# Kernel optimization log

Measured on AMD Instinct MI355X. Metric: run time of the kernel, lower is better.

## Reference

```python
import jax, jax.numpy as jnp
import numpy as np

N = 100000   # nodes
E = 1600000  # edges (before self-loops)
HIDDEN = 256
BN_EPS = 1e-5


def setup_inputs() -> dict:
    key = jax.random.key(0)
    ks = jax.random.split(key, 16)
    def lin(k, i, o):
        return jax.random.normal(k, (i, o), jnp.float32) / np.float32(np.sqrt(i))
    inp = {
        "x": jax.random.normal(ks[0], (N, 21), jnp.float32),
        "edge_index": jax.random.randint(ks[1], (2, E), 0, N),
        # GCNConv weights (stored [in, out]) + biases
        "W1": lin(ks[2], 21, HIDDEN), "b1": jnp.zeros((HIDDEN,), jnp.float32),
        "W2": lin(ks[3], HIDDEN, 112), "b2": jnp.zeros((112,), jnp.float32),
        # dense MLP
        "lin2_w": lin(ks[4], 112, 256), "lin2_b": jnp.zeros((256,), jnp.float32),
        "lin3_w": lin(ks[5], 256, 100), "lin3_b": jnp.zeros((100,), jnp.float32),
        "lin4_w": lin(ks[6], 100, 1),   "lin4_b": jnp.zeros((1,), jnp.float32),
        # batchnorm affine params
        "g1": jnp.ones((112,), jnp.float32), "be1": jnp.zeros((112,), jnp.float32),
        "g2": jnp.ones((256,), jnp.float32), "be2": jnp.zeros((256,), jnp.float32),
        "g3": jnp.ones((100,), jnp.float32), "be3": jnp.zeros((100,), jnp.float32),
    }
    return inp


def _gcn_conv(x, W, b, src, dst, n):
    # PyG GCNConv: h = xW; out_i = sum_j norm_ij * h_j (+ bias), sym-normalized w/ self-loops
    h = x @ W                                              # [N, C]
    deg = jax.ops.segment_sum(jnp.ones(src.shape, h.dtype), dst, num_segments=n)
    dinv = jnp.where(deg > 0, jax.lax.rsqrt(deg), 0.0)
    norm = dinv[src] * dinv[dst]                            # [E']
    out = jax.ops.segment_sum(h[src] * norm[:, None], dst, num_segments=n)
    return out + b


def _bn(x, g, b):
    # train-mode batchnorm: biased batch variance
    m = jnp.mean(x, axis=0)
    v = jnp.mean(jnp.square(x - m), axis=0)
    return (x - m) * jax.lax.rsqrt(v + BN_EPS) * g + b


def reference(x, edge_index, W1, b1, W2, b2, lin2_w, lin2_b, lin3_w, lin3_b,
              lin4_w, lin4_b, g1, be1, g2, be2, g3, be3):
    n = x.shape[0]
    loops = jnp.arange(n, dtype=edge_index.dtype)
    src = jnp.concatenate([edge_index[0], loops])
    dst = jnp.concatenate([edge_index[1], loops])
    h = jax.nn.relu(_gcn_conv(x, W1, b1, src, dst, n))
    h = _gcn_conv(h, W2, b2, src, dst, n)
    h = jax.nn.relu(_bn(h, g1, be1))
    # dropout: identity (eval / deterministic)
    h = jax.nn.relu(_bn(h @ lin2_w + lin2_b, g2, be2))
    h = jax.nn.relu(_bn(h @ lin3_w + lin3_b, g3, be3))
    return h @ lin4_w + lin4_b
```

## Files before the change

### kernel.cpp

```cpp
#include <hip/hip_runtime.h>

#define N_NODES 100000
#define N_EDGES 1600000

typedef _Float16 f16x8 __attribute__((ext_vector_type(8)));
typedef _Float16 f16x4 __attribute__((ext_vector_type(4)));
typedef float fx4 __attribute__((ext_vector_type(4)));

#define NREP 16
#define NBUCK 196
#define CHUNK 8192
#define BCAP 12288

__global__ __launch_bounds__(256) void k_bin(const int* __restrict__ ei,
                                             unsigned* __restrict__ binned,
                                             int* __restrict__ gcount) {
  __shared__ unsigned pr[CHUNK];
  __shared__ unsigned srt[CHUNK];
  __shared__ unsigned char bk[CHUNK];
  __shared__ int hist[256], scanb[256], offs[256], bs[256], gb[256];
  const int t = threadIdx.x;
  const int e0 = blockIdx.x * CHUNK;
  const int n = min(CHUNK, N_EDGES - e0);
  hist[t] = 0;
  __syncthreads();
  for (int i = t; i < n; i += 256) {
    int src = ei[e0 + i], dst = ei[N_EDGES + e0 + i];
    int b = dst >> 9;
    pr[i] = ((unsigned)src << 9) | (unsigned)(dst & 511);
    bk[i] = (unsigned char)b;
    atomicAdd(&hist[b], 1);
  }
  __syncthreads();
  int v = hist[t];
  scanb[t] = v;
  __syncthreads();
  for (int off = 1; off < 256; off <<= 1) {
    int a = (t >= off) ? scanb[t - off] : 0;
    __syncthreads();
    scanb[t] += a;
    __syncthreads();
  }
  offs[t] = scanb[t] - v;
  bs[t] = scanb[t] - v;
  __syncthreads();
  for (int i = t; i < n; i += 256) {
    int b = bk[i];
    int p = atomicAdd(&offs[b], 1);
    srt[p] = pr[i];
  }
  if (t < NBUCK && v > 0) gb[t] = atomicAdd(&gcount[t], v);
  __syncthreads();
  int wave = t >> 6, lane = t & 63;
  for (int b = wave; b < NBUCK; b += 4) {
    int c = hist[b];
    if (c == 0) continue;
    int ls = bs[b], base = gb[b];
    unsigned* dstp = binned + (size_t)b * BCAP + base;
    for (int i = lane; i < c; i += 64) dstp[i] = srt[ls + i];
  }
}

__global__ void k_bscan(const int* __restrict__ gcount, int* __restrict__ gbase) {
  __shared__ int s[256];
  int t = threadIdx.x;
  int v = (t < NBUCK) ? gcount[t] : 0;
  s[t] = v;
  __syncthreads();
  for (int off = 1; off < 256; off <<= 1) {
    int a = (t >= off) ? s[t - off] : 0;
    __syncthreads();
    s[t] += a;
    __syncthreads();
  }
  if (t < NBUCK) gbase[t] = s[t] - v;
}

__global__ __launch_bounds__(256) void k_csr(const unsigned* __restrict__ binned,
                                             const int* __restrict__ gcount,
                                             const int* __restrict__ gbase,
                                             int* __restrict__ rowoff,
                                             int* __restrict__ cnt,
                                             float* __restrict__ dinv,
                                             int* __restrict__ csr) {
  __shared__ int hist[512], offs[512], ps[256];
  __shared__ unsigned srt[BCAP];
  const int b = blockIdx.x, t = threadIdx.x;
  const int n = min(gcount[b], BCAP);
  const int gb0 = gbase[b];
  const unsigned* bp = binned + (size_t)b * BCAP;
  hist[t] = 0;
  hist[t + 256] = 0;
  __syncthreads();
  for (int i = t; i < n; i += 256) atomicAdd(&hist[bp[i] & 511], 1);
  __syncthreads();
  int e0v = hist[2 * t], e1v = hist[2 * t + 1];
  ps[t] = e0v + e1v;
  __syncthreads();
  for (int off = 1; off < 256; off <<= 1) {
    int a = (t >= off) ? ps[t - off] : 0;
    __syncthreads();
    ps[t] += a;
    __syncthreads();
  }
  int excl = ps[t] - (e0v + e1v);
  offs[2 * t] = excl;
  offs[2 * t + 1] = excl + e0v;
  __syncthreads();
#pragma unroll
  for (int u = 0; u < 2; ++u) {
    int j = 2 * t + u;
    int nd = (b << 9) + j;
    if (nd < N_NODES) {
      int c = hist[j];
      cnt[nd] = c;
      dinv[nd] = rsqrtf((float)(c + 1));
      rowoff[nd] = gb0 + offs[j];
    }
  }
  __syncthreads();
  for (int i = t; i < n; i += 256) {
    unsigned p = bp[i];
    int d = p & 511;
    int pos = atomicAdd(&offs[d], 1);
    srt[pos] = p >> 9;
  }
  __syncthreads();
  for (int i = t; i < n; i += 256) csr[gb0 + i] = (int)srt[i];
}

__global__ void k_xpad(const float* __restrict__ x, const float* __restrict__ dinv,
                       float* __restrict__ xs) {
  int idx = blockIdx.x * 256 + threadIdx.x;
  if (idx >= N_NODES * 24) return;
  int r = idx / 24, c = idx - r * 24;
  xs[idx] = (c < 21) ? x[r * 21 + c] * dinv[r] : 0.f;
}

__global__ __launch_bounds__(256) void k_aggx(
    const float4* __restrict__ xs4, const float* __restrict__ dinv,
    const int* __restrict__ rowoff, const int* __restrict__ cnt,
    const int* __restrict__ csr, float4* __restrict__ aggx4) {
  int lane = threadIdx.x & 63, wave = threadIdx.x >> 6;
  int j = lane / 6, c4 = lane - j * 6;
  if (j >= 10) return;
  int i = blockIdx.x * 40 + wave * 10 + j;
  float di = dinv[i];
  int start = rowoff[i], len = cnt[i];
  float4 a0 = xs4[i * 6 + c4];
  float4 a1 = make_float4(0.f, 0.f, 0.f, 0.f);
  int e = 0;
  for (; e + 1 < len; e += 2) {
    int s0 = csr[start + e], s1 = csr[start + e + 1];
    float4 u0 = xs4[s0 * 6 + c4];
    float4 u1 = xs4[s1 * 6 + c4];
    a0.x += u0.x; a0.y += u0.y; a0.z += u0.z; a0.w += u0.w;
    a1.x += u1.x; a1.y += u1.y; a1.z += u1.z; a1.w += u1.w;
  }
  if (e < len) {
    int s0 = csr[start + e];
    float4 u0 = xs4[s0 * 6 + c4];
    a0.x += u0.x; a0.y += u0.y; a0.z += u0.z; a0.w += u0.w;
  }
  float4 r;
  r.x = di * (a0.x + a1.x); r.y = di * (a0.y + a1.y);
  r.z = di * (a0.z + a1.z); r.w = di * (a0.w + a1.w);
  aggx4[i * 6 + c4] = r;
}

__global__ __launch_bounds__(256) void k_gemm1(const float4* __restrict__ aggx4,
                                               const float* __restrict__ W1,
                                               const float* __restrict__ b1,
                                               _Float16* __restrict__ h1) {
  __shared__ float As[32][24];
  int t = threadIdx.x;
  int base = blockIdx.x * 32;
  for (int idx = t; idx < 32 * 6; idx += 256) {
    int m = idx / 6, q = idx - m * 6;
    *(float4*)(&As[m][q * 4]) = aggx4[(base + m) * 6 + q];
  }
  float w[21];
#pragma unroll
  for (int k = 0; k < 21; ++k) w[k] = W1[k * 256 + t];
  float bias = b1[t];
  __syncthreads();
  for (int m = 0; m < 32; ++m) {
    float acc = bias;
#pragma unroll
    for (int k = 0; k < 21; ++k) acc = fmaf(As[m][k], w[k], acc);
    h1[(size_t)(base + m) * 256 + t] = (_Float16)fmaxf(acc, 0.f);
  }
}

template <int K, int KPAD, int NOUT, int NR>
__global__ void k_wcvt(const float* __restrict__ W, _Float16* __restrict__ Wh) {
  int idx = blockIdx.x * 256 + threadIdx.x;
  if (idx >= NR * KPAD) return;
  int n = idx / KPAD, k = idx % KPAD;
  float v = (n < NOUT && k < K) ? W[k * NOUT + n] : 0.f;
  Wh[idx] = (_Float16)v;
}

template <int K, int KPAD, int NT, int MT, int WR, int WC, int MINW,
          bool BN, bool STATS, bool F16IN, bool F16OUT>
__global__ __launch_bounds__(256, MINW) void k_mgemm(
    const void* __restrict__ Av, const _Float16* __restrict__ Wt,
    const float* __restrict__ bias, const float* __restrict__ bn_a,
    const float* __restrict__ bn_c, const float* __restrict__ rowscale,
    void* __restrict__ Cv, int NOUTr, float* __restrict__ sums,
    float* __restrict__ sqs) {
  constexpr int BM = WR * MT * 16;
  constexpr int NR = WC * NT * 16;
  constexpr int BKP = 40;
  constexpr int NC = KPAD / 32;
  constexpr int AIT = BM * 4 / 256;
  constexpr int ABYTES = BM * BKP * 2;
  constexpr int BBYTES = NR * BKP * 2;
  __shared__ __align__(16) char smem[ABYTES + BBYTES];
  _Float16* Ah = (_Float16*)smem;
  _Float16* Bh = (_Float16*)(smem + ABYTES);
  const float* A32 = (const float*)Av;
  const _Float16* A16 = (const _Float16*)Av;
  float* C = (float*)Cv;
  _Float16* C16 = (_Float16*)Cv;

  const int tid = threadIdx.x;
  const int lane = tid & 63, wave = tid >> 6;
  const int wr = wave % WR, wc = wave / WR;
  const int quad = lane >> 4, ln = lane & 15;
  const int rowbase = blockIdx.x * BM;

  fx4 acc[MT][NT];
#pragma unroll
  for (int mt = 0; mt < MT; ++mt)
#pragma unroll
    for (int j = 0; j < NT; ++j) acc[mt][j] = (fx4){0.f, 0.f, 0.f, 0.f};

  f16x8 pf16[AIT];
  fx4 pf32a[AIT], pf32b[AIT];

  auto loadA = [&](int kc) {
#pragma unroll
    for (int it = 0; it < AIT; ++it) {
      int idx = tid + it * 256;
      int m = idx >> 2, q = idx & 3;
      int gi = rowbase + m;
      int k = kc * 32 + q * 8;
      bool ok = (gi < N_NODES) && (k < K);
      if constexpr (F16IN) {
        f16x8 z;
#pragma unroll
        for (int t = 0; t < 8; ++t) z[t] = (_Float16)0;
        pf16[it] = ok ? *(const f16x8*)(A16 + (size_t)gi * K + k) : z;
      } else {
        if (ok) {
          pf32a[it] = *(const fx4*)(A32 + (size_t)gi * K + k);
          pf32b[it] = *(const fx4*)(A32 + (size_t)gi * K + k + 4);
        } else {
          pf32a[it] = (fx4){0.f, 0.f, 0.f, 0.f};
          pf32b[it] = (fx4){0.f, 0.f, 0.f, 0.f};
        }
      }
    }
  };

  auto writeA = [&](int kc) {
#pragma unroll
    for (int it = 0; it < AIT; ++it) {
      int idx = tid + it * 256;
      int m = idx >> 2, q = idx & 3;
      int k = kc * 32 + q * 8;
      float vv[8];
      if constexpr (F16IN) {
#pragma unroll
        for (int t = 0; t < 8; ++t) vv[t] = (float)pf16[it][t];
      } else {
#pragma unroll
        for (int t = 0; t < 4; ++t) { vv[t] = pf32a[it][t]; vv[t + 4] = pf32b[it][t]; }
      }
      if constexpr (BN) {
        if (k < K) {
          float4 a0 = *(const float4*)(bn_a + k);
          float4 a1 = *(const float4*)(bn_a + k + 4);
          float4 c0 = *(const float4*)(bn_c + k);
          float4 c1 = *(const float4*)(bn_c + k + 4);
          float av[8] = {a0.x, a0.y, a0.z, a0.w, a1.x, a1.y, a1.z, a1.w};
          float cv[8] = {c0.x, c0.y, c0.z, c0.w, c1.x, c1.y, c1.z, c1.w};
#pragma unroll
          for (int t = 0; t < 8; ++t) vv[t] = fmaxf(fmaf(vv[t], av[t], cv[t]), 0.f);
        }
      }
      f16x8 hv;
#pragma unroll
      for (int t = 0; t < 8; ++t) hv[t] = (_Float16)vv[t];
      *(f16x8*)(Ah + m * BKP + q * 8) = hv;
    }
  };

  loadA(0);
  for (int kc = 0; kc < NC; ++kc) {
    __syncthreads();
    writeA(kc);
    for (int idx = tid; idx < NR * 4; idx += 256) {
      int n = idx >> 2, p = idx & 3;
      *(f16x8*)(Bh + n * BKP + p * 8) =
          *(const f16x8*)(Wt + n * KPAD + kc * 32 + p * 8);
    }
    __syncthreads();
    if (kc + 1 < NC) loadA(kc + 1);
    f16x8 nf[MT];
#pragma unroll
    for (int mt = 0; mt < MT; ++mt) {
      int r = (wr * MT + mt) * 16 + ln;
      nf[mt] = *(const f16x8*)(Ah + r * BKP + quad * 8);
    }
#pragma unroll
    for (int j = 0; j < NT; ++j) {
      int n = (wc * NT + j) * 16 + ln;
      f16x8 wh = *(const f16x8*)(Bh + n * BKP + quad * 8);
#pragma unroll
      for (int mt = 0; mt < MT; ++mt)
        acc[mt][j] = __builtin_amdgcn_mfma_f32_16x16x32_f16(wh, nf[mt], acc[mt][j], 0, 0, 0);
    }
  }

  float* s_s = (float*)smem;
  float* s_q = s_s + NR;
  __syncthreads();
  if constexpr (STATS) {
    for (int c = tid; c < 2 * NR; c += 256) s_s[c] = 0.f;
    __syncthreads();
  }
  float rs[MT];
#pragma unroll
  for (int mt = 0; mt < MT; ++mt) {
    int nd = rowbase + (wr * MT + mt) * 16 + ln;
    rs[mt] = (rowscale != nullptr && nd < N_NODES) ? rowscale[nd] : 1.f;
  }
#pragma unroll
  for (int j = 0; j < NT; ++j) {
    int ch0 = (wc * NT + j) * 16 + quad * 4;
    bool cv = ch0 < NOUTr;
    float4 b4 = make_float4(0.f, 0.f, 0.f, 0.f);
    if (cv && bias != nullptr) b4 = *(const float4*)(bias + ch0);
    float sc[4] = {0.f, 0.f, 0.f, 0.f}, sq[4] = {0.f, 0.f, 0.f, 0.f};
#pragma unroll
    for (int mt = 0; mt < MT; ++mt) {
      int nd = rowbase + (wr * MT + mt) * 16 + ln;
      if (nd < N_NODES && cv) {
        float v0 = (acc[mt][j][0] + b4.x) * rs[mt];
        float v1 = (acc[mt][j][1] + b4.y) * rs[mt];
        float v2 = (acc[mt][j][2] + b4.z) * rs[mt];
        float v3 = (acc[mt][j][3] + b4.w) * rs[mt];
        if constexpr (F16OUT) {
          f16x4 o = {(_Float16)v0, (_Float16)v1, (_Float16)v2, (_Float16)v3};
          *(f16x4*)(C16 + (size_t)nd * NOUTr + ch0) = o;
        } else {
          float4 o = make_float4(v0, v1, v2, v3);
          *(float4*)(C + (size_t)nd * NOUTr + ch0) = o;
        }
        if constexpr (STATS) {
          sc[0] += v0; sq[0] = fmaf(v0, v0, sq[0]);
          sc[1] += v1; sq[1] = fmaf(v1, v1, sq[1]);
          sc[2] += v2; sq[2] = fmaf(v2, v2, sq[2]);
          sc[3] += v3; sq[3] = fmaf(v3, v3, sq[3]);
        }
      }
    }
    if constexpr (STATS) {
      if (cv) {
#pragma unroll
        for (int r = 0; r < 4; ++r) {
          float s = sc[r], q = sq[r];
          s += __shfl_xor(s, 1); q += __shfl_xor(q, 1);
          s += __shfl_xor(s, 2); q += __shfl_xor(q, 2);
          s += __shfl_xor(s, 4); q += __shfl_xor(q, 4);
          s += __shfl_xor(s, 8); q += __shfl_xor(q, 8);
          if (ln == 0) {
            atomicAdd(&s_s[ch0 + r], s);
            atomicAdd(&s_q[ch0 + r], q);
          }
        }
      }
    }
  }
  if constexpr (STATS) {
    __syncthreads();
    int rep = (blockIdx.x & (NREP - 1));
    for (int c = tid; c < NR; c += 256) {
      if (c < NOUTr) {
        atomicAdd(&sums[rep * NOUTr + c], s_s[c]);
        atomicAdd(&sqs[rep * NOUTr + c], s_q[c]);
      }
    }
  }
}

__global__ __launch_bounds__(256) void k_agg2(
    const f16x8* __restrict__ t2s8, const float* __restrict__ dinv,
    const int* __restrict__ rowoff, const int* __restrict__ cnt,
    const int* __restrict__ csr, const float* __restrict__ b2,
    _Float16* __restrict__ g2) {
  int lane = threadIdx.x & 63, wave = threadIdx.x >> 6;
  int j = lane / 14, c = lane - j * 14;
  if (j >= 4) return;
  int i = blockIdx.x * 16 + wave * 4 + j;
  float di = dinv[i];
  int start = rowoff[i], len = cnt[i];
  f16x8 u = t2s8[i * 14 + c];
  fx4 a0, a1, b0, b1;
#pragma unroll
  for (int t = 0; t < 4; ++t) { a0[t] = (float)u[t]; b0[t] = (float)u[t + 4]; }
  a1 = (fx4){0.f, 0.f, 0.f, 0.f};
  b1 = (fx4){0.f, 0.f, 0.f, 0.f};
  int e = 0;
  for (; e + 1 < len; e += 2) {
    int s0 = csr[start + e], s1 = csr[start + e + 1];
    f16x8 u0 = t2s8[s0 * 14 + c];
    f16x8 u1 = t2s8[s1 * 14 + c];
#pragma unroll
    for (int t = 0; t < 4; ++t) {
      a0[t] += (float)u0[t]; b0[t] += (float)u0[t + 4];
      a1[t] += (float)u1[t]; b1[t] += (float)u1[t + 4];
    }
  }
  if (e < len) {
    int s0 = csr[start + e];
    f16x8 u0 = t2s8[s0 * 14 + c];
#pragma unroll
    for (int t = 0; t < 4; ++t) { a0[t] += (float)u0[t]; b0[t] += (float)u0[t + 4]; }
  }
  float4 blo = *(const float4*)(b2 + c * 8);
  float4 bhi = *(const float4*)(b2 + c * 8 + 4);
  f16x8 o;
  o[0] = (_Float16)fmaf(di, a0[0] + a1[0], blo.x);
  o[1] = (_Float16)fmaf(di, a0[1] + a1[1], blo.y);
  o[2] = (_Float16)fmaf(di, a0[2] + a1[2], blo.z);
  o[3] = (_Float16)fmaf(di, a0[3] + a1[3], blo.w);
  o[4] = (_Float16)fmaf(di, b0[0] + b1[0], bhi.x);
  o[5] = (_Float16)fmaf(di, b0[1] + b1[1], bhi.y);
  o[6] = (_Float16)fmaf(di, b0[2] + b1[2], bhi.z);
  o[7] = (_Float16)fmaf(di, b0[3] + b1[3], bhi.w);
  *(f16x8*)(g2 + (size_t)i * 112 + c * 8) = o;
}

template <int C>
__global__ void k_colstats16(const _Float16* __restrict__ X, float* __restrict__ sums,
                             float* __restrict__ sqs) {
  int c = threadIdx.x;
  if (c >= C) return;
  int chunk = (N_NODES + gridDim.x - 1) / gridDim.x;
  int i0 = blockIdx.x * chunk;
  int i1 = min(N_NODES, i0 + chunk);
  float s = 0.f, q = 0.f;
  for (int i = i0; i < i1; ++i) {
    float v = (float)X[(size_t)i * C + c];
    s += v;
    q = fmaf(v, v, q);
  }
  int rep = (blockIdx.x & (NREP - 1));
  atomicAdd(&sums[rep * C + c], s);
  atomicAdd(&sqs[rep * C + c], q);
}

template <int C>
__global__ void k_bnfinal(const float* __restrict__ sums, const float* __restrict__ sqs,
                          const float* __restrict__ gamma, const float* __restrict__ beta,
                          float* __restrict__ bn_a, float* __restrict__ bn_c) {
  int c = threadIdx.x;
  if (c >= C) return;
  float s = 0.f, q = 0.f;
#pragma unroll
  for (int r = 0; r < NREP; ++r) {
    s += sums[r * C + c];
    q += sqs[r * C + c];
  }
  const float inv_n = 1.0f / (float)N_NODES;
  float mean = s * inv_n;
  float var = fmaxf(q * inv_n - mean * mean, 0.f);
  float rstd = 1.0f / sqrtf(var + 1e-5f);
  float a = gamma[c] * rstd;
  bn_a[c] = a;
  bn_c[c] = beta[c] - mean * a;
}

__global__ void k_final(const float* __restrict__ h4, const float* __restrict__ bn_a,
                        const float* __restrict__ bn_c, const float* __restrict__ w4,
                        const float* __restrict__ b4, float* __restrict__ out) {
  int lane = threadIdx.x & 63;
  int i = blockIdx.x * 4 + (threadIdx.x >> 6);
  float acc = fmaxf(fmaf(h4[(size_t)i * 100 + lane], bn_a[lane], bn_c[lane]), 0.f) * w4[lane];
  if (lane < 36) {
    int k = lane + 64;
    acc += fmaxf(fmaf(h4[(size_t)i * 100 + k], bn_a[k], bn_c[k]), 0.f) * w4[k];
  }
#pragma unroll
  for (int off = 32; off >= 1; off >>= 1) acc += __shfl_down(acc, off);
  if (lane == 0) out[i] = acc + b4[0];
}

extern "C" void kernel_launch(void* const* d_in, const int* in_sizes, int n_in,
                              void* d_out, int out_size, void* d_ws, size_t ws_size,
                              hipStream_t stream) {
  const float* x   = (const float*)d_in[0];
  const int*   ei  = (const int*)d_in[1];
  const float* W1  = (const float*)d_in[2];
  const float* b1  = (const float*)d_in[3];
  const float* W2  = (const float*)d_in[4];
  const float* b2  = (const float*)d_in[5];
  const float* l2w = (const float*)d_in[6];
  const float* l2b = (const float*)d_in[7];
  const float* l3w = (const float*)d_in[8];
  const float* l3b = (const float*)d_in[9];
  const float* l4w = (const float*)d_in[10];
  const float* l4b = (const float*)d_in[11];
  const float* g1  = (const float*)d_in[12];
  const float* be1 = (const float*)d_in[13];
  const float* g2w = (const float*)d_in[14];
  const float* be2 = (const float*)d_in[15];
  const float* g3  = (const float*)d_in[16];
  const float* be3 = (const float*)d_in[17];
  float* out = (float*)d_out;

  char* base = (char*)d_ws;
  size_t off = 0;
  auto alloc = [&](size_t bytes) -> char* {
    char* p = base + off;
    off = (off + bytes + 255) & ~(size_t)255;
    return p;
  };
  int*   cnt    = (int*)alloc((size_t)N_NODES * 4);
  int*   rowoff = (int*)alloc((size_t)N_NODES * 4);
  float* dinv   = (float*)alloc((size_t)N_NODES * 4);
  int*   csr    = (int*)alloc((size_t)N_EDGES * 4);
  unsigned* binned = (unsigned*)alloc((size_t)NBUCK * BCAP * 4);
  int*   gcount = (int*)alloc(NBUCK * 4);
  int*   gbase  = (int*)alloc(NBUCK * 4);
  float* stats  = (float*)alloc((size_t)NREP * 960 * 4);
  float* bnco   = (float*)alloc(960 * 4);
  float* xs     = (float*)alloc((size_t)N_NODES * 24 * 4);
  float* aggx   = (float*)alloc((size_t)N_NODES * 24 * 4);
  _Float16* h1  = (_Float16*)alloc((size_t)N_NODES * 256 * 2);
  _Float16* t2s = (_Float16*)alloc((size_t)N_NODES * 112 * 2);
  _Float16* g2h = (_Float16*)alloc((size_t)N_NODES * 112 * 2);
  float* h4     = (float*)alloc((size_t)N_NODES * 112 * 4);
  _Float16* wt2 = (_Float16*)alloc(112 * 256 * 2);
  _Float16* wt3 = (_Float16*)alloc(256 * 128 * 2);
  _Float16* wt4 = (_Float16*)alloc(112 * 256 * 2);

  float* sums1 = stats;
  float* sqs1  = sums1 + NREP * 112;
  float* sums2 = sqs1 + NREP * 112;
  float* sqs2  = sums2 + NREP * 256;
  float* sums3 = sqs2 + NREP * 256;
  float* sqs3  = sums3 + NREP * 112;
  float* bn_a1 = bnco + 0,   *bn_c1 = bnco + 112;
  float* bn_a2 = bnco + 224, *bn_c2 = bnco + 480;
  float* bn_a3 = bnco + 736, *bn_c3 = bnco + 848;

  hipMemsetAsync(gcount, 0, NBUCK * 4, stream);
  hipMemsetAsync(stats, 0, (size_t)NREP * 960 * 4, stream);

  k_bin<<<NBUCK, 256, 0, stream>>>(ei, binned, gcount);
  k_bscan<<<1, 256, 0, stream>>>(gcount, gbase);
  k_csr<<<NBUCK, 256, 0, stream>>>(binned, gcount, gbase, rowoff, cnt, dinv, csr);

  k_wcvt<256, 256, 112, 112><<<112, 256, 0, stream>>>(W2, wt2);
  k_wcvt<112, 128, 256, 256><<<128, 256, 0, stream>>>(l2w, wt3);
  k_wcvt<256, 256, 100, 112><<<112, 256, 0, stream>>>(l3w, wt4);

  k_xpad<<<(N_NODES * 24 + 255) / 256, 256, 0, stream>>>(x, dinv, xs);
  k_aggx<<<2500, 256, 0, stream>>>((const float4*)xs, dinv, rowoff, cnt, csr,
                                   (float4*)aggx);
  k_gemm1<<<3125, 256, 0, stream>>>((const float4*)aggx, W1, b1, h1);

  k_mgemm<256, 256, 7, 2, 4, 1, 4, false, false, true, true><<<782, 256, 0, stream>>>(
      h1, wt2, nullptr, nullptr, nullptr, dinv, t2s, 112, nullptr, nullptr);
  k_agg2<<<6250, 256, 0, stream>>>((const f16x8*)t2s, dinv, rowoff, cnt, csr, b2,
                                   g2h);

  k_colstats16<112><<<1600, 128, 0, stream>>>(g2h, sums1, sqs1);
  k_bnfinal<112><<<1, 128, 0, stream>>>(sums1, sqs1, g1, be1, bn_a1, bn_c1);

  k_mgemm<112, 128, 8, 2, 2, 2, 4, true, true, true, true><<<1563, 256, 0, stream>>>(
      g2h, wt3, l2b, bn_a1, bn_c1, nullptr, h1, 256, sums2, sqs2);
  k_bnfinal<256><<<1, 256, 0, stream>>>(sums2, sqs2, g2w, be2, bn_a2, bn_c2);

  k_mgemm<256, 256, 7, 2, 4, 1, 4, true, true, true, false><<<782, 256, 0, stream>>>(
      h1, wt4, l3b, bn_a2, bn_c2, nullptr, h4, 100, sums3, sqs3);
  k_bnfinal<100><<<1, 128, 0, stream>>>(sums3, sqs3, g3, be3, bn_a3, bn_c3);

  k_final<<<25000, 256, 0, stream>>>(h4, bn_a3, bn_c3, l4w, l4b, out);
}
```

Baseline: 435.1 us.

## Store scaled input features in fp16 and widen gather unroll in aggregations

The padded, dinv-scaled input features are now stored as fp16, so each node row is 48 bytes read as three 16-byte vectors instead of six float4s. This halves the bytes gathered per edge in the first aggregation and lets each wave cover 21 nodes instead of 10. Both gather kernels (first-layer aggregation and second-layer aggregation) now use four independent accumulators and four outstanding loads per iteration to raise memory-level parallelism. The cost is reduced precision on the input features and higher register use per thread.

```diff
diff --git a/kernel.cpp b/kernel.cpp
--- a/kernel.cpp
+++ b/kernel.cpp
@@ -130,42 +130,59 @@
 }
 
 __global__ void k_xpad(const float* __restrict__ x, const float* __restrict__ dinv,
-                       float* __restrict__ xs) {
+                       _Float16* __restrict__ xs) {
   int idx = blockIdx.x * 256 + threadIdx.x;
   if (idx >= N_NODES * 24) return;
   int r = idx / 24, c = idx - r * 24;
-  xs[idx] = (c < 21) ? x[r * 21 + c] * dinv[r] : 0.f;
+  xs[idx] = (_Float16)((c < 21) ? x[r * 21 + c] * dinv[r] : 0.f);
 }
 
 __global__ __launch_bounds__(256) void k_aggx(
-    const float4* __restrict__ xs4, const float* __restrict__ dinv,
+    const f16x8* __restrict__ xs3, const float* __restrict__ dinv,
     const int* __restrict__ rowoff, const int* __restrict__ cnt,
-    const int* __restrict__ csr, float4* __restrict__ aggx4) {
+    const int* __restrict__ csr, float* __restrict__ aggx) {
   int lane = threadIdx.x & 63, wave = threadIdx.x >> 6;
-  int j = lane / 6, c4 = lane - j * 6;
-  if (j >= 10) return;
-  int i = blockIdx.x * 40 + wave * 10 + j;
+  int j = lane / 3, c = lane - j * 3;
+  if (j >= 21) return;
+  int i = blockIdx.x * 84 + wave * 21 + j;
+  if (i >= N_NODES) return;
   float di = dinv[i];
   int start = rowoff[i], len = cnt[i];
-  float4 a0 = xs4[i * 6 + c4];
-  float4 a1 = make_float4(0.f, 0.f, 0.f, 0.f);
+  f16x8 u = xs3[i * 3 + c];
+  float a0[8], a1[8], a2[8], a3[8];
+#pragma unroll
+  for (int t = 0; t < 8; ++t) { a0[t] = (float)u[t]; a1[t] = a2[t] = a3[t] = 0.f; }
   int e = 0;
-  for (; e + 1 < len; e += 2) {
+  for (; e + 3 < len; e += 4) {
     int s0 = csr[start + e], s1 = csr[start + e + 1];
-    float4 u0 = xs4[s0 * 6 + c4];
-    float4 u1 = xs4[s1 * 6 + c4];
-    a0.x += u0.x; a0.y += u0.y; a0.z += u0.z; a0.w += u0.w;
-    a1.x += u1.x; a1.y += u1.y; a1.z += u1.z; a1.w += u1.w;
-  }
-  if (e < len) {
+    int s2 = csr[start + e + 2], s3 = csr[start + e + 3];
+    f16x8 u0 = xs3[s0 * 3 + c];
+    f16x8 u1 = xs3[s1 * 3 + c];
+    f16x8 u2 = xs3[s2 * 3 + c];
+    f16x8 u3 = xs3[s3 * 3 + c];
+#pragma unroll
+    for (int t = 0; t < 8; ++t) {
+      a0[t] += (float)u0[t]; a1[t] += (float)u1[t];
+      a2[t] += (float)u2[t]; a3[t] += (float)u3[t];
+    }
+  }
+  for (; e < len; ++e) {
     int s0 = csr[start + e];
-    float4 u0 = xs4[s0 * 6 + c4];
-    a0.x += u0.x; a0.y += u0.y; a0.z += u0.z; a0.w += u0.w;
-  }
-  float4 r;
-  r.x = di * (a0.x + a1.x); r.y = di * (a0.y + a1.y);
-  r.z = di * (a0.z + a1.z); r.w = di * (a0.w + a1.w);
-  aggx4[i * 6 + c4] = r;
+    f16x8 u0 = xs3[s0 * 3 + c];
+#pragma unroll
+    for (int t = 0; t < 8; ++t) a0[t] += (float)u0[t];
+  }
+  float4 r0, r1;
+  r0.x = di * (a0[0] + a1[0] + a2[0] + a3[0]);
+  r0.y = di * (a0[1] + a1[1] + a2[1] + a3[1]);
+  r0.z = di * (a0[2] + a1[2] + a2[2] + a3[2]);
+  r0.w = di * (a0[3] + a1[3] + a2[3] + a3[3]);
+  r1.x = di * (a0[4] + a1[4] + a2[4] + a3[4]);
+  r1.y = di * (a0[5] + a1[5] + a2[5] + a3[5]);
+  r1.z = di * (a0[6] + a1[6] + a2[6] + a3[6]);
+  r1.w = di * (a0[7] + a1[7] + a2[7] + a3[7]);
+  *(float4*)(aggx + (size_t)i * 24 + c * 8) = r0;
+  *(float4*)(aggx + (size_t)i * 24 + c * 8 + 4) = r1;
 }
 
 __global__ __launch_bounds__(256) void k_gemm1(const float4* __restrict__ aggx4,
@@ -408,39 +425,36 @@
   float di = dinv[i];
   int start = rowoff[i], len = cnt[i];
   f16x8 u = t2s8[i * 14 + c];
-  fx4 a0, a1, b0, b1;
-#pragma unroll
-  for (int t = 0; t < 4; ++t) { a0[t] = (float)u[t]; b0[t] = (float)u[t + 4]; }
-  a1 = (fx4){0.f, 0.f, 0.f, 0.f};
-  b1 = (fx4){0.f, 0.f, 0.f, 0.f};
+  float a0[8], a1[8], a2[8], a3[8];
+#pragma unroll
+  for (int t = 0; t < 8; ++t) { a0[t] = (float)u[t]; a1[t] = a2[t] = a3[t] = 0.f; }
   int e = 0;
-  for (; e + 1 < len; e += 2) {
+  for (; e + 3 < len; e += 4) {
     int s0 = csr[start + e], s1 = csr[start + e + 1];
+    int s2 = csr[start + e + 2], s3 = csr[start + e + 3];
     f16x8 u0 = t2s8[s0 * 14 + c];
     f16x8 u1 = t2s8[s1 * 14 + c];
-#pragma unroll
-    for (int t = 0; t < 4; ++t) {
-      a0[t] += (float)u0[t]; b0[t] += (float)u0[t + 4];
-      a1[t] += (float)u1[t]; b1[t] += (float)u1[t + 4];
-    }
-  }
-  if (e < len) {
+    f16x8 u2 = t2s8[s2 * 14 + c];
+    f16x8 u3 = t2s8[s3 * 14 + c];
+#pragma unroll
+    for (int t = 0; t < 8; ++t) {
+      a0[t] += (float)u0[t]; a1[t] += (float)u1[t];
+      a2[t] += (float)u2[t]; a3[t] += (float)u3[t];
+    }
+  }
+  for (; e < len; ++e) {
     int s0 = csr[start + e];
     f16x8 u0 = t2s8[s0 * 14 + c];
 #pragma unroll
-    for (int t = 0; t < 4; ++t) { a0[t] += (float)u0[t]; b0[t] += (float)u0[t + 4]; }
+    for (int t = 0; t < 8; ++t) a0[t] += (float)u0[t];
   }
   float4 blo = *(const float4*)(b2 + c * 8);
   float4 bhi = *(const float4*)(b2 + c * 8 + 4);
+  float bb[8] = {blo.x, blo.y, blo.z, blo.w, bhi.x, bhi.y, bhi.z, bhi.w};
   f16x8 o;
-  o[0] = (_Float16)fmaf(di, a0[0] + a1[0], blo.x);
-  o[1] = (_Float16)fmaf(di, a0[1] + a1[1], blo.y);
-  o[2] = (_Float16)fmaf(di, a0[2] + a1[2], blo.z);
-  o[3] = (_Float16)fmaf(di, a0[3] + a1[3], blo.w);
-  o[4] = (_Float16)fmaf(di, b0[0] + b1[0], bhi.x);
-  o[5] = (_Float16)fmaf(di, b0[1] + b1[1], bhi.y);
-  o[6] = (_Float16)fmaf(di, b0[2] + b1[2], bhi.z);
-  o[7] = (_Float16)fmaf(di, b0[3] + b1[3], bhi.w);
+#pragma unroll
+  for (int t = 0; t < 8; ++t)
+    o[t] = (_Float16)fmaf(di, a0[t] + a1[t] + a2[t] + a3[t], bb[t]);
   *(f16x8*)(g2 + (size_t)i * 112 + c * 8) = o;
 }
 
@@ -538,7 +552,7 @@
   int*   gbase  = (int*)alloc(NBUCK * 4);
   float* stats  = (float*)alloc((size_t)NREP * 960 * 4);
   float* bnco   = (float*)alloc(960 * 4);
-  float* xs     = (float*)alloc((size_t)N_NODES * 24 * 4);
+  _Float16* xs  = (_Float16*)alloc((size_t)N_NODES * 24 * 2);
   float* aggx   = (float*)alloc((size_t)N_NODES * 24 * 4);
   _Float16* h1  = (_Float16*)alloc((size_t)N_NODES * 256 * 2);
   _Float16* t2s = (_Float16*)alloc((size_t)N_NODES * 112 * 2);
@@ -570,8 +584,8 @@
   k_wcvt<256, 256, 100, 112><<<112, 256, 0, stream>>>(l3w, wt4);
 
   k_xpad<<<(N_NODES * 24 + 255) / 256, 256, 0, stream>>>(x, dinv, xs);
-  k_aggx<<<2500, 256, 0, stream>>>((const float4*)xs, dinv, rowoff, cnt, csr,
-                                   (float4*)aggx);
+  k_aggx<<<(N_NODES + 83) / 84, 256, 0, stream>>>((const f16x8*)xs, dinv, rowoff,
+                                                  cnt, csr, aggx);
   k_gemm1<<<3125, 256, 0, stream>>>((const float4*)aggx, W1, b1, h1);
 
   k_mgemm<256, 256, 7, 2, 4, 1, 4, false, false, true, true><<<782, 256, 0, stream>>>(
```

Result: faster. 414.8 us (-4.7%).
